# Optimization experiments

Hardware: AMD Instinct MI355X
Metric: run time of the kernel (lower is better)

The kernel has to match this reference:

```python
import jax, jax.numpy as jnp
import numpy as np

B, DIM, H, W = 8, 128, 192, 192
HEADS = 4
WS = 8        # window size
SHIFT = 4     # shift size
N = WS * WS   # tokens per window
HD = DIM // HEADS
NW = (H // WS) * (W // WS)


def _relative_position_index(ws):
    coords = np.stack(np.meshgrid(np.arange(ws), np.arange(ws), indexing='ij'))  # (2,ws,ws)
    cf = coords.reshape(2, -1)                                                   # (2,N)
    rel = cf[:, :, None] - cf[:, None, :]                                        # (2,N,N)
    rel = rel.transpose(1, 2, 0).astype(np.int64)                                # (N,N,2)
    rel[:, :, 0] += ws - 1
    rel[:, :, 1] += ws - 1
    rel[:, :, 0] *= 2 * ws - 1
    return rel.sum(-1)  # (N,N)


def _window_partition_np(x, ws):
    b, h, w, c = x.shape
    x = x.reshape(b, h // ws, ws, w // ws, ws, c)
    return x.transpose(0, 1, 3, 2, 4, 5).reshape(-1, ws, ws, c)


def _shift_mask(h, w, ws, shift):
    img_mask = np.zeros((1, h, w, 1), dtype=np.float32)
    slices = (slice(0, -ws), slice(-ws, -shift), slice(-shift, None))
    cnt = 0
    for hs in slices:
        for wsl in slices:
            img_mask[:, hs, wsl, :] = cnt
            cnt += 1
    mw = _window_partition_np(img_mask, ws).reshape(-1, ws * ws)  # (nW, N)
    attn_mask = mw[:, None, :] - mw[:, :, None]                    # (nW, N, N)
    return np.where(attn_mask != 0, -100.0, 0.0).astype(np.float32)


_RPI = jnp.asarray(_relative_position_index(WS))   # (N,N) int
_MASK = jnp.asarray(_shift_mask(H, W, WS, SHIFT))  # (nW,N,N)


def setup_inputs() -> dict:
    key = jax.random.key(0)
    k0, k1, k2, k3 = jax.random.split(key, 4)
    return {
        'x': jax.random.normal(k0, (B, DIM, H, W), jnp.float32),
        'qkv_w': jax.random.normal(k1, (3 * DIM, DIM), jnp.float32) * 0.02,
        'qkv_b': jnp.zeros((3 * DIM,), jnp.float32),
        'proj_w': jax.random.normal(k2, (DIM, DIM), jnp.float32) * 0.02,
        'proj_b': jnp.zeros((DIM,), jnp.float32),
        'rpb_table': jax.random.normal(k3, ((2 * WS - 1) ** 2, HEADS), jnp.float32) * 0.02,
    }


def reference(x, qkv_w, qkv_b, proj_w, proj_b, rpb_table):
    scale = HD ** -0.5
    # (B,C,H,W) -> (B,H,W,C)
    xs = jnp.transpose(x, (0, 2, 3, 1))
    # cyclic shift
    xs = jnp.roll(xs, shift=(-SHIFT, -SHIFT), axis=(1, 2))
    # window partition -> (B*nW, N, C)
    win = xs.reshape(B, H // WS, WS, W // WS, WS, DIM)
    win = jnp.transpose(win, (0, 1, 3, 2, 4, 5)).reshape(B * NW, N, DIM)
    # qkv projection
    qkv = win @ qkv_w.T + qkv_b                                   # (B_,N,3C)
    qkv = qkv.reshape(B * NW, N, 3, HEADS, HD)
    qkv = jnp.transpose(qkv, (2, 0, 3, 1, 4))                     # (3,B_,h,N,d)
    q, k, v = qkv[0], qkv[1], qkv[2]
    attn = jnp.einsum('bhnd,bhmd->bhnm', q * scale, k)            # (B_,h,N,N)
    # relative position bias
    bias = rpb_table[_RPI.reshape(-1)].reshape(N, N, HEADS)
    bias = jnp.transpose(bias, (2, 0, 1))                         # (h,N,N)
    attn = attn + bias[None]
    # shift mask per window
    attn = attn.reshape(B, NW, HEADS, N, N) + _MASK[None, :, None]
    attn = jax.nn.softmax(attn.reshape(B * NW, HEADS, N, N), axis=-1)
    out = jnp.einsum('bhnm,bhmd->bhnd', attn, v)                  # (B_,h,N,d)
    out = jnp.transpose(out, (0, 2, 1, 3)).reshape(B * NW, N, DIM)
    out = out @ proj_w.T + proj_b
    # window reverse -> (B,H,W,C)
    out = out.reshape(B, H // WS, W // WS, WS, WS, DIM)
    out = jnp.transpose(out, (0, 1, 3, 2, 4, 5)).reshape(B, H, W, DIM)
    # reverse cyclic shift
    out = jnp.roll(out, shift=(SHIFT, SHIFT), axis=(1, 2))
    return jnp.transpose(out, (0, 3, 1, 2))  # (B,C,H,W)
```

## Files before the change

kernel.cpp:

```cpp
#include <hip/hip_runtime.h>

#define HIMG 192
#define HWSZ (192*192)
#define NWX  24

typedef __bf16 bf16;
typedef __bf16 bf16x2 __attribute__((ext_vector_type(2)));
typedef __bf16 bf16x4 __attribute__((ext_vector_type(4)));
typedef __bf16 bf16x8 __attribute__((ext_vector_type(8)));
typedef float  f32x4  __attribute__((ext_vector_type(4)));

#define MFMA(a,b,c) __builtin_amdgcn_mfma_f32_16x16x32_bf16((a),(b),(c),0,0,0)
#define SW(r) (((((r)&7) ^ ((((r)>>3)&1)<<2))) << 4)

static __device__ __forceinline__ bf16x8 ldg8(const float* p) {
    const float4 u = ((const float4*)p)[0];
    const float4 v = ((const float4*)p)[1];
    bf16x8 r;
    r[0]=(bf16)u.x; r[1]=(bf16)u.y; r[2]=(bf16)u.z; r[3]=(bf16)u.w;
    r[4]=(bf16)v.x; r[5]=(bf16)v.y; r[6]=(bf16)v.z; r[7]=(bf16)v.w;
    return r;
}
template<int WSB>
static __device__ __forceinline__ bf16x8 ldw(const float* wf, const bf16* wh, int off) {
    if (WSB) return *(const bf16x8*)(wh + off);
    return ldg8(wf + off);
}
static __device__ __forceinline__ bf16x4 pk4b(f32x4 v, float4 b) {
    bf16x4 r; r[0]=(bf16)(v[0]+b.x); r[1]=(bf16)(v[1]+b.y);
    r[2]=(bf16)(v[2]+b.z); r[3]=(bf16)(v[3]+b.w); return r;
}
static __device__ __forceinline__ bf16x4 pk4bs(f32x4 v, float4 b, float s) {
    bf16x4 r; r[0]=(bf16)((v[0]+b.x)*s); r[1]=(bf16)((v[1]+b.y)*s);
    r[2]=(bf16)((v[2]+b.z)*s); r[3]=(bf16)((v[3]+b.w)*s); return r;
}
static __device__ __forceinline__ bf16x4 pk4c(f32x4 v, float b) {
    bf16x4 r; r[0]=(bf16)(v[0]+b); r[1]=(bf16)(v[1]+b);
    r[2]=(bf16)(v[2]+b); r[3]=(bf16)(v[3]+b); return r;
}
static __device__ __forceinline__ bf16x4 pk4s(f32x4 v, float s) {
    bf16x4 r; r[0]=(bf16)(v[0]*s); r[1]=(bf16)(v[1]*s);
    r[2]=(bf16)(v[2]*s); r[3]=(bf16)(v[3]*s); return r;
}
static __device__ __forceinline__ bf16x4 pk4(f32x4 v) {
    bf16x4 r; r[0]=(bf16)v[0]; r[1]=(bf16)v[1]; r[2]=(bf16)v[2]; r[3]=(bf16)v[3]; return r;
}
static __device__ __forceinline__ bf16x8 cat8(bf16x4 a, bf16x4 b) {
    bf16x8 r; r[0]=a[0]; r[1]=a[1]; r[2]=a[2]; r[3]=a[3];
    r[4]=b[0]; r[5]=b[1]; r[6]=b[2]; r[7]=b[3]; return r;
}
static __device__ __forceinline__ f32x4 splat4(float b) {
    f32x4 r; r[0]=b; r[1]=b; r[2]=b; r[3]=b; return r;
}
static __device__ __forceinline__ f32x4 f4of(float4 b) {
    f32x4 r; r[0]=b.x; r[1]=b.y; r[2]=b.z; r[3]=b.w; return r;
}
static __device__ __forceinline__ f32x4 f4ofs(float4 b, float s) {
    f32x4 r; r[0]=b.x*s; r[1]=b.y*s; r[2]=b.z*s; r[3]=b.w*s; return r;
}

__global__ __launch_bounds__(256) void setup_ws(const float* __restrict__ rpb,
                                                const float* __restrict__ qkv_w,
                                                const float* __restrict__ proj_w,
                                                float* __restrict__ wbias,
                                                bf16* __restrict__ hqkv,
                                                bf16* __restrict__ hproj,
                                                float* __restrict__ wbf,
                                                bf16* __restrict__ hqkvf,
                                                bf16* __restrict__ hprojf) {
    const int e = blockIdx.x * 256 + threadIdx.x;
    if (e < 16384) {
        const int h = e >> 12, i = (e >> 6) & 63, j = e & 63;
        const int dy = (i >> 3) - (j >> 3) + 7;
        const int dx = (i & 7)  - (j & 7)  + 7;
        wbias[e] = rpb[(dy * 15 + dx) * 4 + h];
    } else if (e < 65536) {
        const int i = e - 16384;
        hqkv[i] = (bf16)qkv_w[i];
    } else if (e < 81920) {
        const int i = e - 65536;
        hproj[i] = (bf16)proj_w[i];
    } else if (e < 98304) {
        const int t = e - 81920;
        const int r = t & 3, lane = (t >> 2) & 63;
        const int m = (t >> 8) & 3, n = (t >> 10) & 3, h = t >> 12;
        const int lo = lane & 15, hi = lane >> 4;
        const int i_ = n*16 + lo;
        const int j_ = (m >> 1)*32 + hi*8 + (m & 1)*4 + r;
        const int dy = (i_ >> 3) - (j_ >> 3) + 7;
        const int dx = (i_ & 7)  - (j_ & 7)  + 7;
        wbf[t] = rpb[(dy * 15 + dx) * 4 + h];
    } else if (e < 147456) {
        const int t = e - 98304;
        const int el = t & 7, lane = (t >> 3) & 63;
        const int a = (t >> 9) & 1, kb = (t >> 10) & 3;
        const int h = (t >> 12) & 3, ph = t >> 14;
        const int lo = lane & 15, hi = lane >> 4;
        const int prow = ((lo >> 2) << 3) + (lo & 3);
        const int row = (ph == 2) ? (256 + h*32 + a*16 + lo)
                                  : (ph*128 + h*32 + prow + a*4);
        const int col = kb*32 + hi*8 + el;
        float wv_ = qkv_w[row*128 + col];
        if (ph == 0) wv_ *= 0.17677669529663687f;
        hqkvf[t] = (bf16)wv_;
    } else {
        const int t = e - 147456;
        const int el = t & 7, lane = (t >> 3) & 63;
        const int tA = (t >> 9) & 3, kb = (t >> 11) & 3, oh = t >> 13;
        const int lo = lane & 15, hi = lane >> 4;
        const int row = oh*64 + tA*16 + lo;
        const int col = kb*32 + hi*8 + el;
        hprojf[t] = (bf16)proj_w[row*128 + col];
    }
}

__global__ __launch_bounds__(512, 2)
void xform(const float* __restrict__ x, bf16* __restrict__ xw)
{
    __shared__ char sT[8 * 3088];
    const int tid   = threadIdx.x;
    const int bid   = blockIdx.x;
    const int batch = bid & 7;
    const int co    = (bid >> 3) & 15;
    const int wy    = bid >> 7;

    #pragma unroll
    for (int k = 0; k < 3; ++k) {
        const int idx = tid + k*512;
        const int chp = idx / 384;
        const int rem = idx - chp*384;
        const int c4  = rem >> 3;
        const int row = rem & 7;
        int hr = wy*8 + row + 4; if (hr >= HIMG) hr -= HIMG;
        const float* p0 = x + (size_t)(batch*128 + co*8 + chp*2) * HWSZ
                          + hr*HIMG + c4*4;
        const float4 a = *(const float4*)p0;
        const float4 b = *(const float4*)(p0 + HWSZ);
        int cw0 = c4*4 - 4; if (cw0 < 0) cw0 += HIMG;
        #pragma unroll
        for (int e = 0; e < 4; ++e) {
            const int cw = cw0 + e;
            const int entry = cw ^ ((cw >> 2) & 3);
            bf16x2 pr; pr[0] = (bf16)(&a.x)[e]; pr[1] = (bf16)(&b.x)[e];
            *(bf16x2*)(sT + row*3088 + entry*16 + chp*4) = pr;
        }
    }
    __syncthreads();

    #pragma unroll
    for (int j = 0; j < 3; ++j) {
        const int otok = tid + j*512;
        const int wxx = otok >> 6;
        const int t   = otok & 63;
        const int iy  = t >> 3, ix = t & 7;
        const int cw  = wxx*8 + ix;
        const int entry = cw ^ ((cw >> 2) & 3);
        const bf16x8 v = *(const bf16x8*)(sT + iy*3088 + entry*16);
        const int win = (wy*NWX + wxx)*8 + batch;
        *(bf16x8*)(xw + (size_t)win*8192 + co*512 + t*8) = v;
    }
}

__global__ __launch_bounds__(256, 3)
void qkv_attn(const bf16* __restrict__ xw, const float* __restrict__ qkv_b,
              const bf16* __restrict__ hqkvf, const float* __restrict__ wbf,
              bf16* __restrict__ obuf)
{
    const int tid  = threadIdx.x;
    const int lane = tid & 63;
    const int h    = tid >> 6;
    const int lo   = lane & 15;
    const int hi   = lane >> 4;

    const int bid   = blockIdx.x;
    const int wrem  = bid >> 3;
    const int wy    = wrem / NWX;
    const int wx    = wrem - wy * NWX;

    const f32x4 FZ = {0.f, 0.f, 0.f, 0.f};
    const float SCALE = 0.17677669529663687f;
    const int prow = ((lo >> 2) << 3) + (lo & 3);

    const bf16* const xwb = xw + (size_t)bid * 8192;
    const bf16* const wQ = hqkvf + h * 4096;
    const bf16* const wK = hqkvf + 16384 + h * 4096;
    const bf16* const wV = hqkvf + 32768 + h * 4096;

    bf16x8 qf[4], kf[4], vf[2][2];

    {
        const float4 b0 = *(const float4*)(qkv_b + h*32 + hi*8);
        const float4 b1 = *(const float4*)(qkv_b + h*32 + hi*8 + 4);
        const f32x4 c0 = f4ofs(b0, SCALE);
        const f32x4 c1 = f4ofs(b1, SCALE);
        f32x4 acc[2][4];
        #pragma unroll
        for (int n = 0; n < 4; ++n) { acc[0][n] = c0; acc[1][n] = c1; }
        #pragma unroll
        for (int kb = 0; kb < 4; ++kb) {
            bf16x8 xf[4];
            #pragma unroll
            for (int n = 0; n < 4; ++n)
                xf[n] = *(const bf16x8*)(xwb + (kb*4 + hi)*512 + (n*16 + lo)*8);
            const bf16x8 w0 = *(const bf16x8*)(wQ + (kb*2    )*512 + lane*8);
            const bf16x8 w1 = *(const bf16x8*)(wQ + (kb*2 + 1)*512 + lane*8);
            #pragma unroll
            for (int n = 0; n < 4; ++n) {
                acc[0][n] = MFMA(w0, xf[n], acc[0][n]);
                acc[1][n] = MFMA(w1, xf[n], acc[1][n]);
            }
        }
        #pragma unroll
        for (int n = 0; n < 4; ++n)
            qf[n] = cat8(pk4(acc[0][n]), pk4(acc[1][n]));
    }

    {
        const float4 k0 = *(const float4*)(qkv_b + 128 + h*32 + hi*8);
        const float4 k1 = *(const float4*)(qkv_b + 128 + h*32 + hi*8 + 4);
        const float bv0 = qkv_b[256 + h*32 + lo];
        const float bv1 = qkv_b[256 + h*32 + 16 + lo];
        const f32x4 ck0 = f4of(k0), ck1 = f4of(k1);
        const f32x4 cv0 = splat4(bv0), cv1 = splat4(bv1);
        f32x4 ak[2][4], av[4][2];
        #pragma unroll
        for (int m = 0; m < 4; ++m) {
            ak[0][m] = ck0; ak[1][m] = ck1; av[m][0] = cv0; av[m][1] = cv1;
        }
        #pragma unroll
        for (int kb = 0; kb < 4; ++kb) {
            bf16x8 xf[4];
            #pragma unroll
            for (int m = 0; m < 4; ++m) {
                const int row = (m >> 1)*32 + (m & 1)*4 + prow;
                xf[m] = *(const bf16x8*)(xwb + (kb*4 + hi)*512 + row*8);
            }
            const bf16x8 wk0 = *(const bf16x8*)(wK + (kb*2    )*512 + lane*8);
            const bf16x8 wk1 = *(const bf16x8*)(wK + (kb*2 + 1)*512 + lane*8);
            const bf16x8 wv0 = *(const bf16x8*)(wV + (kb*2    )*512 + lane*8);
            const bf16x8 wv1 = *(const bf16x8*)(wV + (kb*2 + 1)*512 + lane*8);
            #pragma unroll
            for (int m = 0; m < 4; ++m) {
                ak[0][m] = MFMA(wk0, xf[m], ak[0][m]);
                ak[1][m] = MFMA(wk1, xf[m], ak[1][m]);
                av[m][0] = MFMA(xf[m], wv0, av[m][0]);
                av[m][1] = MFMA(xf[m], wv1, av[m][1]);
            }
        }
        #pragma unroll
        for (int m = 0; m < 4; ++m)
            kf[m] = cat8(pk4(ak[0][m]), pk4(ak[1][m]));
        #pragma unroll
        for (int kb = 0; kb < 2; ++kb) {
            vf[0][kb] = cat8(pk4(av[kb*2][0]), pk4(av[kb*2 + 1][0]));
            vf[1][kb] = cat8(pk4(av[kb*2][1]), pk4(av[kb*2 + 1][1]));
        }
    }

    const bool ey = (wy == 23), ex = (wx == 23);
    const bool edge = ey || ex;
    const float* const wbh = wbf + h * 4096;
    bf16x8 pf[2][4];
    float rinv[4];
    #pragma unroll
    for (int n = 0; n < 4; ++n) {
        const int i_ = n*16 + lo;
        const int yi = i_ >> 3, xi = i_ & 7;
        const int ri = (ey ? (yi < 4 ? 1 : 2) : 0) * 3 + (ex ? (xi < 4 ? 1 : 2) : 0);
        f32x4 sc[4];
        #pragma unroll
        for (int m = 0; m < 4; ++m) {
            f32x4 ci = *(const f32x4*)(wbh + (n*4 + m)*256 + lane*4);
            if (edge) {
                #pragma unroll
                for (int r = 0; r < 4; ++r) {
                    const int j_ = (m >> 1)*32 + hi*8 + (m & 1)*4 + r;
                    const int yj = j_ >> 3, xj = j_ & 7;
                    const int rj = (ey ? (yj < 4 ? 1 : 2) : 0) * 3 + (ex ? (xj < 4 ? 1 : 2) : 0);
                    ci[r] += (ri != rj) ? -100.0f : 0.0f;
                }
            }
            sc[m] = MFMA(kf[m], qf[n], ci);
        }
        float sum = 0.f;
        #pragma unroll
        for (int m = 0; m < 4; ++m)
            #pragma unroll
            for (int r = 0; r < 4; ++r) {
                const float p = __expf(sc[m][r]);
                sc[m][r] = p; sum += p;
            }
        sum += __shfl_xor(sum, 16);
        sum += __shfl_xor(sum, 32);
        rinv[n] = 1.0f / sum;
        pf[0][n] = cat8(pk4(sc[0]), pk4(sc[1]));
        pf[1][n] = cat8(pk4(sc[2]), pk4(sc[3]));
    }

    f32x4 o0[2][4];
    #pragma unroll
    for (int o = 0; o < 2; ++o)
        #pragma unroll
        for (int n = 0; n < 4; ++n) o0[o][n] = FZ;
    #pragma unroll
    for (int kb = 0; kb < 2; ++kb)
        #pragma unroll
        for (int o = 0; o < 2; ++o)
            #pragma unroll
            for (int n = 0; n < 4; ++n)
                o0[o][n] = MFMA(vf[o][kb], pf[kb][n], o0[o][n]);

    bf16* const ob = obuf + (size_t)bid * 8192 + h * 2048;
    #pragma unroll
    for (int n = 0; n < 4; ++n)
        #pragma unroll
        for (int o = 0; o < 2; ++o)
            *(bf16x4*)(ob + (n*2 + o)*256 + lane*4) = pk4s(o0[o][n], rinv[n]);
}

__global__ __launch_bounds__(512, 3)
void proj_rows(const bf16* __restrict__ obuf, const bf16* __restrict__ hprojf,
               const float* __restrict__ proj_b, float* __restrict__ out)
{
    __shared__ char sR[49152];
    const int tid  = threadIdx.x;
    const int lane = tid & 63;
    const int wv   = tid >> 6;
    const int lo   = lane & 15;
    const int hi   = lane >> 4;

    const int bid   = blockIdx.x;
    const int batch = bid & 7;
    const int hh    = bid >> 3;
    int hr = hh + 188; if (hr >= 192) hr -= 192;
    const int wy = hr >> 3, iy = hr & 7;
    const int n_ = iy >> 1;

    #pragma unroll
    for (int k = 0; k < 6; ++k) {
        const int i  = tid + k*512;
        const int wr = i >> 4;
        const int cc = i & 15;
        const int wxx = wr >> 3, ix = wr & 7;
        const int win = (wy*NWX + wxx)*8 + batch;
        const int lo2 = (iy & 1)*8 + ix;
        const int hg = cc >> 2, oo = (cc >> 1) & 1, hp = cc & 1;
        const bf16* bp = obuf + (size_t)win*8192 + hg*2048 + (n_*2 + oo)*256;
        const bf16x4 p0 = *(const bf16x4*)(bp + ((hp*2    )*16 + lo2)*4);
        const bf16x4 p1 = *(const bf16x4*)(bp + ((hp*2 + 1)*16 + lo2)*4);
        int wo = wr + 4; if (wo >= 192) wo -= 192;
        *(bf16x8*)(sR + wo*256 + ((cc*16) ^ SW(wo))) = cat8(p0, p1);
    }
    __syncthreads();

    const int q  = wv >> 1;
    const int oh = wv & 1;
    const f32x4 FZ = {0.f, 0.f, 0.f, 0.f};
    f32x4 acc[4][3];
    #pragma unroll
    for (int tA = 0; tA < 4; ++tA)
        #pragma unroll
        for (int tN = 0; tN < 3; ++tN) acc[tA][tN] = FZ;

    #pragma unroll
    for (int kb = 0; kb < 4; ++kb) {
        bf16x8 of[3];
        #pragma unroll
        for (int tN = 0; tN < 3; ++tN) {
            const int tok = q*48 + tN*16 + lo;
            of[tN] = *(const bf16x8*)(sR + tok*256 + ((kb*64 + hi*16) ^ SW(tok)));
        }
        bf16x8 wf[4];
        #pragma unroll
        for (int tA = 0; tA < 4; ++tA)
            wf[tA] = *(const bf16x8*)(hprojf + (size_t)(((oh*4 + kb)*4 + tA)*64 + lane)*8);
        #pragma unroll
        for (int tA = 0; tA < 4; ++tA)
            #pragma unroll
            for (int tN = 0; tN < 3; ++tN)
                acc[tA][tN] = MFMA(of[tN], wf[tA], acc[tA][tN]);
    }

    #pragma unroll
    for (int tA = 0; tA < 4; ++tA) {
        const int oc = oh*64 + tA*16 + lo;
        const float pb = proj_b[oc];
        float* const orow = out + (size_t)(batch*128 + oc) * HWSZ + hh*HIMG;
        #pragma unroll
        for (int tN = 0; tN < 3; ++tN) {
            const int tb = q*48 + tN*16 + hi*4;
            float4 v;
            v.x = acc[tA][tN][0] + pb;
            v.y = acc[tA][tN][1] + pb;
            v.z = acc[tA][tN][2] + pb;
            v.w = acc[tA][tN][3] + pb;
            *(float4*)(orow + tb) = v;
        }
    }
}

template<int WSB>
__global__ __launch_bounds__(64, 2)
void swin_fused(const float* __restrict__ x, const float* __restrict__ qkv_w,
                const float* __restrict__ qkv_b, const float* __restrict__ proj_w,
                const float* __restrict__ proj_b, const float* __restrict__ rpb,
                const float* __restrict__ wb, const bf16* __restrict__ hqkv,
                const bf16* __restrict__ hproj, float* __restrict__ out)
{
    __shared__ char sX[16384];

    const int lane = threadIdx.x & 63;
    const int lo   = lane & 15;
    const int hi   = lane >> 4;

    const int bid   = blockIdx.x;
    const int batch = bid & 7;
    const int wrem  = bid >> 3;
    const int wy    = wrem / NWX;
    const int wx    = wrem - wy * NWX;
    const long xbase = (long)batch * 128 * HWSZ;

    const f32x4 FZ = {0.f, 0.f, 0.f, 0.f};
    const float SCALE = 0.17677669529663687f;
    const int prow = ((lo >> 2) << 3) + (lo & 3);

    {
        int hh = wy*8 + (lane >> 3) + 4; if (hh >= HIMG) hh -= HIMG;
        int ww = wx*8 + (lane & 7)  + 4; if (ww >= HIMG) ww -= HIMG;
        const float* xp = x + xbase + hh * HIMG + ww;
        char* const wp = sX + lane * 256;
        const int swz = SW(lane);
        #pragma unroll
        for (int g = 0; g < 16; ++g) {
            bf16x8 v;
            #pragma unroll
            for (int e = 0; e < 8; ++e) v[e] = (bf16)xp[(g*8 + e) * HWSZ];
            *(bf16x8*)(wp + ((16*g) ^ swz)) = v;
        }
    }

    const bool ey = (wy == 23), ex = (wx == 23);
    const bool edge = ey || ex;

    bf16x4 ob[4][2][4];

    #pragma unroll
    for (int h = 0; h < 4; ++h) {
        bf16x8 qf[4], kf[4];
        {
            f32x4 acc[2][4];
            #pragma unroll
            for (int a = 0; a < 2; ++a)
                #pragma unroll
                for (int n = 0; n < 4; ++n) acc[a][n] = FZ;
            #pragma unroll
            for (int kb = 0; kb < 4; ++kb) {
                bf16x8 xf[4];
                #pragma unroll
                for (int n = 0; n < 4; ++n) {
                    const int row = n*16 + lo;
                    xf[n] = *(const bf16x8*)(sX + row*256 + ((kb*64 + hi*16) ^ SW(row)));
                }
                const int coff = kb*32 + hi*8;
                const bf16x8 w0 = ldw<WSB>(qkv_w, hqkv, (h*32 + prow    ) * 128 + coff);
                const bf16x8 w1 = ldw<WSB>(qkv_w, hqkv, (h*32 + prow + 4) * 128 + coff);
                #pragma unroll
                for (int n = 0; n < 4; ++n) {
                    acc[0][n] = MFMA(w0, xf[n], acc[0][n]);
                    acc[1][n] = MFMA(w1, xf[n], acc[1][n]);
                }
            }
            const float4 b0 = *(const float4*)(qkv_b + h*32 + hi*8);
            const float4 b1 = *(const float4*)(qkv_b + h*32 + hi*8 + 4);
            #pragma unroll
            for (int n = 0; n < 4; ++n)
                qf[n] = cat8(pk4bs(acc[0][n], b0, SCALE), pk4bs(acc[1][n], b1, SCALE));
        }
        {
            f32x4 ak[2][4];
            #pragma unroll
            for (int a = 0; a < 2; ++a)
                #pragma unroll
                for (int m = 0; m < 4; ++m) ak[a][m] = FZ;
            #pragma unroll
            for (int kb = 0; kb < 4; ++kb) {
                bf16x8 xf[4];
                #pragma unroll
                for (int m = 0; m < 4; ++m) {
                    const int row = (m >> 1)*32 + (m & 1)*4 + prow;
                    xf[m] = *(const bf16x8*)(sX + row*256 + ((kb*64 + hi*16) ^ SW(row)));
                }
                const int coff = kb*32 + hi*8;
                const bf16x8 w0 = ldw<WSB>(qkv_w, hqkv, (128 + h*32 + prow    ) * 128 + coff);
                const bf16x8 w1 = ldw<WSB>(qkv_w, hqkv, (128 + h*32 + prow + 4) * 128 + coff);
                #pragma unroll
                for (int m = 0; m < 4; ++m) {
                    ak[0][m] = MFMA(w0, xf[m], ak[0][m]);
                    ak[1][m] = MFMA(w1, xf[m], ak[1][m]);
                }
            }
            const float4 b0 = *(const float4*)(qkv_b + 128 + h*32 + hi*8);
            const float4 b1 = *(const float4*)(qkv_b + 128 + h*32 + hi*8 + 4);
            #pragma unroll
            for (int m = 0; m < 4; ++m)
                kf[m] = cat8(pk4b(ak[0][m], b0), pk4b(ak[1][m], b1));
        }

        f32x4 s2[4][4];
        const float* wbh = wb + h * 4096;
        #pragma unroll
        for (int n = 0; n < 4; ++n) {
            const int i_ = n*16 + lo;
            const int yi = i_ >> 3, xi = i_ & 7;
            const int ri = (ey ? (yi < 4 ? 1 : 2) : 0) * 3 + (ex ? (xi < 4 ? 1 : 2) : 0);
            #pragma unroll
            for (int m = 0; m < 4; ++m) {
                const int j0 = (m >> 1)*32 + hi*8 + (m & 1)*4;
                f32x4 ci;
                if (WSB) ci = *(const f32x4*)(wbh + i_*64 + j0);
                else {
                    #pragma unroll
                    for (int r = 0; r < 4; ++r) {
                        const int j_ = j0 + r;
                        ci[r] = rpb[((yi - (j_ >> 3) + 7) * 15 + (xi - (j_ & 7) + 7)) * 4 + h];
                    }
                }
                if (edge) {
                    #pragma unroll
                    for (int r = 0; r < 4; ++r) {
                        const int j_ = j0 + r;
                        const int yj = j_ >> 3, xj = j_ & 7;
                        const int rj = (ey ? (yj < 4 ? 1 : 2) : 0) * 3 + (ex ? (xj < 4 ? 1 : 2) : 0);
                        ci[r] += (ri != rj) ? -100.0f : 0.0f;
                    }
                }
                s2[m][n] = MFMA(kf[m], qf[n], ci);
            }
        }
        float rinv[4];
        #pragma unroll
        for (int n = 0; n < 4; ++n) {
            float mx = -1e30f;
            #pragma unroll
            for (int m = 0; m < 4; ++m)
                #pragma unroll
                for (int r = 0; r < 4; ++r) mx = fmaxf(mx, s2[m][n][r]);
            mx = fmaxf(mx, __shfl_xor(mx, 16));
            mx = fmaxf(mx, __shfl_xor(mx, 32));
            float sum = 0.f;
            #pragma unroll
            for (int m = 0; m < 4; ++m)
                #pragma unroll
                for (int r = 0; r < 4; ++r) {
                    const float p = __expf(s2[m][n][r] - mx);
                    s2[m][n][r] = p; sum += p;
                }
            sum += __shfl_xor(sum, 16);
            sum += __shfl_xor(sum, 32);
            rinv[n] = 1.0f / sum;
        }
        bf16x8 pf[2][4];
        #pragma unroll
        for (int kb = 0; kb < 2; ++kb)
            #pragma unroll
            for (int n = 0; n < 4; ++n)
                pf[kb][n] = cat8(pk4(s2[kb*2][n]), pk4(s2[kb*2 + 1][n]));

        bf16x8 vf[2][2];
        {
            f32x4 av[4][2];
            #pragma unroll
            for (int m = 0; m < 4; ++m) { av[m][0] = FZ; av[m][1] = FZ; }
            #pragma unroll
            for (int kb = 0; kb < 4; ++kb) {
                bf16x8 xv[4];
                #pragma unroll
                for (int m = 0; m < 4; ++m) {
                    const int row = (m >> 1)*32 + (m & 1)*4 + prow;
                    xv[m] = *(const bf16x8*)(sX + row*256 + ((kb*64 + hi*16) ^ SW(row)));
                }
                const int coff = kb*32 + hi*8;
                const bf16x8 w0 = ldw<WSB>(qkv_w, hqkv, (256 + h*32 + lo)      * 128 + coff);
                const bf16x8 w1 = ldw<WSB>(qkv_w, hqkv, (256 + h*32 + 16 + lo) * 128 + coff);
                #pragma unroll
                for (int m = 0; m < 4; ++m) {
                    av[m][0] = MFMA(xv[m], w0, av[m][0]);
                    av[m][1] = MFMA(xv[m], w1, av[m][1]);
                }
            }
            const float bv0 = qkv_b[256 + h*32 + lo];
            const float bv1 = qkv_b[256 + h*32 + 16 + lo];
            #pragma unroll
            for (int kb = 0; kb < 2; ++kb) {
                vf[0][kb] = cat8(pk4c(av[kb*2][0], bv0), pk4c(av[kb*2 + 1][0], bv0));
                vf[1][kb] = cat8(pk4c(av[kb*2][1], bv1), pk4c(av[kb*2 + 1][1], bv1));
            }
        }
        {
            f32x4 o0[2][4];
            #pragma unroll
            for (int o = 0; o < 2; ++o)
                #pragma unroll
                for (int n = 0; n < 4; ++n) o0[o][n] = FZ;
            #pragma unroll
            for (int kb = 0; kb < 2; ++kb)
                #pragma unroll
                for (int o = 0; o < 2; ++o)
                    #pragma unroll
                    for (int n = 0; n < 4; ++n)
                        o0[o][n] = MFMA(vf[o][kb], pf[kb][n], o0[o][n]);
            #pragma unroll
            for (int o = 0; o < 2; ++o)
                #pragma unroll
                for (int n = 0; n < 4; ++n)
                    ob[h][o][n] = pk4s(o0[o][n], rinv[n]);
        }
    }

    #pragma unroll
    for (int h = 0; h < 4; ++h)
        #pragma unroll
        for (int o = 0; o < 2; ++o) {
            const int cb = h*64 + o*32 + hi*8;
            #pragma unroll
            for (int n = 0; n < 4; ++n) {
                const int t = n*16 + lo;
                *(bf16x4*)(sX + t*256 + (cb ^ SW(t))) = ob[h][o][n];
            }
        }

    #pragma unroll
    for (int c4 = 0; c4 < 4; ++c4) {
        f32x4 pr[2][4];
        #pragma unroll
        for (int a = 0; a < 2; ++a)
            #pragma unroll
            for (int n = 0; n < 4; ++n) pr[a][n] = FZ;
        #pragma unroll
        for (int kb = 0; kb < 4; ++kb) {
            bf16x8 af[4];
            #pragma unroll
            for (int n = 0; n < 4; ++n) {
                const int row = n*16 + lo;
                af[n] = *(const bf16x8*)(sX + row*256 + ((kb*64 + hi*16) ^ SW(row)));
            }
            const int coff = kb*32 + hi*8;
            const bf16x8 w0 = ldw<WSB>(proj_w, hproj, (c4*32 + lo)      * 128 + coff);
            const bf16x8 w1 = ldw<WSB>(proj_w, hproj, (c4*32 + 16 + lo) * 128 + coff);
            #pragma unroll
            for (int n = 0; n < 4; ++n) {
                pr[0][n] = MFMA(w0, af[n], pr[0][n]);
                pr[1][n] = MFMA(w1, af[n], pr[1][n]);
            }
        }
        #pragma unroll
        for (int a = 0; a < 2; ++a) {
            const int ocb = c4*32 + a*16 + hi*4;
            const float4 pb = *(const float4*)(proj_b + ocb);
            #pragma unroll
            for (int n = 0; n < 4; ++n) {
                const int t = n*16 + lo;
                int hh = wy*8 + (t >> 3) + 4; if (hh >= HIMG) hh -= HIMG;
                int ww = wx*8 + (t & 7)  + 4; if (ww >= HIMG) ww -= HIMG;
                float* op = out + (long)(batch*128 + ocb) * HWSZ + hh*HIMG + ww;
                op[0]      = pr[a][n][0] + pb.x;
                op[HWSZ]   = pr[a][n][1] + pb.y;
                op[2*HWSZ] = pr[a][n][2] + pb.z;
                op[3*HWSZ] = pr[a][n][3] + pb.w;
            }
        }
    }
}

extern "C" void kernel_launch(void* const* d_in, const int* in_sizes, int n_in,
                              void* d_out, int out_size, void* d_ws, size_t ws_size,
                              hipStream_t stream) {
    const float* x      = (const float*)d_in[0];
    const float* qkv_w  = (const float*)d_in[1];
    const float* qkv_b  = (const float*)d_in[2];
    const float* proj_w = (const float*)d_in[3];
    const float* proj_b = (const float*)d_in[4];
    const float* rpb    = (const float*)d_in[5];
    float* out = (float*)d_out;

    const size_t SETUP = 393216;
    const size_t XWSZ  = (size_t)4608 * 16384;
    const size_t OSZ   = (size_t)4608 * 16384;

    float* wbias = (float*)d_ws;
    bf16*  hqkv  = (bf16*)((char*)d_ws + 65536);
    bf16*  hproj = (bf16*)((char*)d_ws + 163840);
    float* wbf   = (float*)((char*)d_ws + 196608);
    bf16*  hqkvf = (bf16*)((char*)d_ws + 262144);
    bf16*  hprojf= (bf16*)((char*)d_ws + 360448);
    bf16*  xw    = (bf16*)((char*)d_ws + SETUP);
    bf16*  obuf  = (bf16*)((char*)d_ws + SETUP + XWSZ);

    if (ws_size >= SETUP + XWSZ + OSZ) {
        setup_ws<<<640, 256, 0, stream>>>(rpb, qkv_w, proj_w, wbias, hqkv, hproj,
                                          wbf, hqkvf, hprojf);
        xform<<<3072, 512, 0, stream>>>(x, xw);
        qkv_attn<<<4608, 256, 0, stream>>>(xw, qkv_b, hqkvf, wbf, obuf);
        proj_rows<<<1536, 512, 0, stream>>>(obuf, hprojf, proj_b, out);
    } else if (ws_size >= SETUP) {
        setup_ws<<<640, 256, 0, stream>>>(rpb, qkv_w, proj_w, wbias, hqkv, hproj,
                                          wbf, hqkvf, hprojf);
        swin_fused<1><<<4608, 64, 0, stream>>>(x, qkv_w, qkv_b, proj_w, proj_b, rpb,
                                               wbias, hqkv, hproj, out);
    } else {
        swin_fused<0><<<4608, 64, 0, stream>>>(x, qkv_w, qkv_b, proj_w, proj_b, rpb,
                                               nullptr, nullptr, nullptr, out);
    }
}
```

Measured before the change: 180.3 us.

## Fuse shift/window-partition transform into qkv_attn via swizzled LDS staging

Removes the separate xform kernel and its bf16 intermediate buffer. Each qkv_attn block now reads its shifted 8x8 window directly from the fp32 NCHW input, converts it to bf16 and stores it in a swizzled 16KB LDS tile, and the Q/K/V MFMA loops read fragments from LDS instead of global memory. This saves one launch plus a full write and read of the intermediate tensor. In exchange the reads of x are only 16 bytes wide per row segment, and the extra LDS and __syncthreads may lower occupancy.

```diff
diff --git a/kernel.cpp b/kernel.cpp
--- a/kernel.cpp
+++ b/kernel.cpp
@@ -114,58 +114,12 @@
     }
 }
 
-__global__ __launch_bounds__(512, 2)
-void xform(const float* __restrict__ x, bf16* __restrict__ xw)
-{
-    __shared__ char sT[8 * 3088];
-    const int tid   = threadIdx.x;
-    const int bid   = blockIdx.x;
-    const int batch = bid & 7;
-    const int co    = (bid >> 3) & 15;
-    const int wy    = bid >> 7;
-
-    #pragma unroll
-    for (int k = 0; k < 3; ++k) {
-        const int idx = tid + k*512;
-        const int chp = idx / 384;
-        const int rem = idx - chp*384;
-        const int c4  = rem >> 3;
-        const int row = rem & 7;
-        int hr = wy*8 + row + 4; if (hr >= HIMG) hr -= HIMG;
-        const float* p0 = x + (size_t)(batch*128 + co*8 + chp*2) * HWSZ
-                          + hr*HIMG + c4*4;
-        const float4 a = *(const float4*)p0;
-        const float4 b = *(const float4*)(p0 + HWSZ);
-        int cw0 = c4*4 - 4; if (cw0 < 0) cw0 += HIMG;
-        #pragma unroll
-        for (int e = 0; e < 4; ++e) {
-            const int cw = cw0 + e;
-            const int entry = cw ^ ((cw >> 2) & 3);
-            bf16x2 pr; pr[0] = (bf16)(&a.x)[e]; pr[1] = (bf16)(&b.x)[e];
-            *(bf16x2*)(sT + row*3088 + entry*16 + chp*4) = pr;
-        }
-    }
-    __syncthreads();
-
-    #pragma unroll
-    for (int j = 0; j < 3; ++j) {
-        const int otok = tid + j*512;
-        const int wxx = otok >> 6;
-        const int t   = otok & 63;
-        const int iy  = t >> 3, ix = t & 7;
-        const int cw  = wxx*8 + ix;
-        const int entry = cw ^ ((cw >> 2) & 3);
-        const bf16x8 v = *(const bf16x8*)(sT + iy*3088 + entry*16);
-        const int win = (wy*NWX + wxx)*8 + batch;
-        *(bf16x8*)(xw + (size_t)win*8192 + co*512 + t*8) = v;
-    }
-}
-
 __global__ __launch_bounds__(256, 3)
-void qkv_attn(const bf16* __restrict__ xw, const float* __restrict__ qkv_b,
+void qkv_attn(const float* __restrict__ x, const float* __restrict__ qkv_b,
               const bf16* __restrict__ hqkvf, const float* __restrict__ wbf,
               bf16* __restrict__ obuf)
 {
+    __shared__ char sX[16384];
     const int tid  = threadIdx.x;
     const int lane = tid & 63;
     const int h    = tid >> 6;
@@ -173,6 +127,7 @@
     const int hi   = lane >> 4;
 
     const int bid   = blockIdx.x;
+    const int batch = bid & 7;
     const int wrem  = bid >> 3;
     const int wy    = wrem / NWX;
     const int wx    = wrem - wy * NWX;
@@ -181,7 +136,31 @@
     const float SCALE = 0.17677669529663687f;
     const int prow = ((lo >> 2) << 3) + (lo & 3);
 
-    const bf16* const xwb = xw + (size_t)bid * 8192;
+    {
+        const int hbase = wy*8 + 4;
+        const int wbase = wx*8 + 4;
+        #pragma unroll
+        for (int k = 0; k < 4; ++k) {
+            const int id  = k*256 + tid;
+            const int w4  = id & 1;
+            const int row = (id >> 1) & 7;
+            const int chp = id >> 4;
+            int hh = hbase + row;  if (hh >= HIMG) hh -= HIMG;
+            int ww = wbase + w4*4; if (ww >= HIMG) ww -= HIMG;
+            const float* p0 = x + (size_t)(batch*128 + chp*2) * HWSZ + hh*HIMG + ww;
+            const float4 a = *(const float4*)p0;
+            const float4 b = *(const float4*)(p0 + HWSZ);
+            const int t0 = row*8 + w4*4;
+            #pragma unroll
+            for (int e = 0; e < 4; ++e) {
+                const int t = t0 + e;
+                bf16x2 pr; pr[0] = (bf16)(&a.x)[e]; pr[1] = (bf16)(&b.x)[e];
+                *(bf16x2*)(sX + t*256 + ((4*chp) ^ SW(t))) = pr;
+            }
+        }
+    }
+    __syncthreads();
+
     const bf16* const wQ = hqkvf + h * 4096;
     const bf16* const wK = hqkvf + 16384 + h * 4096;
     const bf16* const wV = hqkvf + 32768 + h * 4096;
@@ -200,8 +179,10 @@
         for (int kb = 0; kb < 4; ++kb) {
             bf16x8 xf[4];
             #pragma unroll
-            for (int n = 0; n < 4; ++n)
-                xf[n] = *(const bf16x8*)(xwb + (kb*4 + hi)*512 + (n*16 + lo)*8);
+            for (int n = 0; n < 4; ++n) {
+                const int row = n*16 + lo;
+                xf[n] = *(const bf16x8*)(sX + row*256 + ((kb*64 + hi*16) ^ SW(row)));
+            }
             const bf16x8 w0 = *(const bf16x8*)(wQ + (kb*2    )*512 + lane*8);
             const bf16x8 w1 = *(const bf16x8*)(wQ + (kb*2 + 1)*512 + lane*8);
             #pragma unroll
@@ -233,7 +214,7 @@
             #pragma unroll
             for (int m = 0; m < 4; ++m) {
                 const int row = (m >> 1)*32 + (m & 1)*4 + prow;
-                xf[m] = *(const bf16x8*)(xwb + (kb*4 + hi)*512 + row*8);
+                xf[m] = *(const bf16x8*)(sX + row*256 + ((kb*64 + hi*16) ^ SW(row)));
             }
             const bf16x8 wk0 = *(const bf16x8*)(wK + (kb*2    )*512 + lane*8);
             const bf16x8 wk1 = *(const bf16x8*)(wK + (kb*2 + 1)*512 + lane*8);
@@ -684,7 +665,6 @@
     float* out = (float*)d_out;
 
     const size_t SETUP = 393216;
-    const size_t XWSZ  = (size_t)4608 * 16384;
     const size_t OSZ   = (size_t)4608 * 16384;
 
     float* wbias = (float*)d_ws;
@@ -693,14 +673,12 @@
     float* wbf   = (float*)((char*)d_ws + 196608);
     bf16*  hqkvf = (bf16*)((char*)d_ws + 262144);
     bf16*  hprojf= (bf16*)((char*)d_ws + 360448);
-    bf16*  xw    = (bf16*)((char*)d_ws + SETUP);
-    bf16*  obuf  = (bf16*)((char*)d_ws + SETUP + XWSZ);
-
-    if (ws_size >= SETUP + XWSZ + OSZ) {
+    bf16*  obuf  = (bf16*)((char*)d_ws + SETUP);
+
+    if (ws_size >= SETUP + OSZ) {
         setup_ws<<<640, 256, 0, stream>>>(rpb, qkv_w, proj_w, wbias, hqkv, hproj,
                                           wbf, hqkvf, hprojf);
-        xform<<<3072, 512, 0, stream>>>(x, xw);
-        qkv_attn<<<4608, 256, 0, stream>>>(xw, qkv_b, hqkvf, wbf, obuf);
+        qkv_attn<<<4608, 256, 0, stream>>>(x, qkv_b, hqkvf, wbf, obuf);
         proj_rows<<<1536, 512, 0, stream>>>(obuf, hprojf, proj_b, out);
     } else if (ws_size >= SETUP) {
         setup_ws<<<640, 256, 0, stream>>>(rpb, qkv_w, proj_w, wbias, hqkv, hproj,
```

After: 155.6 us. 1.16x faster.
